# Kernel tuning notes

Hardware: AMD Instinct MI355X
Metric: run time of the kernel (lower is better)

## Reference

```python
import jax, jax.numpy as jnp
import numpy as np

N_HEADS = 16

def setup_inputs() -> dict:
    key = jax.random.key(0)
    k1, k2, k3 = jax.random.split(key, 3)
    B, T, C = 4, 2048, 1024
    x = jax.random.normal(k1, (B, T, C), dtype=jnp.float32)
    tok_mask = jnp.ones((B, T), dtype=bool)
    # weights pre-transposed to [in, out] (torch Linear stores [out, in])
    w_qkv = jax.random.normal(k2, (C, 3 * C), dtype=jnp.float32) * (C ** -0.5)
    w_proj = jax.random.normal(k3, (C, C), dtype=jnp.float32) * (C ** -0.5)
    return {"x": x, "tok_mask": tok_mask, "w_qkv": w_qkv, "w_proj": w_proj}


def reference(x, tok_mask, w_qkv, w_proj):
    B, T, C = x.shape
    H = N_HEADS
    d = C // H
    qkv = x @ w_qkv  # [B, T, 3C]
    q, k, v = jnp.split(qkv, 3, axis=-1)
    # [B, T, C] -> [B, H, T, d]
    def heads(t):
        return t.reshape(B, T, H, d).transpose(0, 2, 1, 3)
    q, k, v = heads(q), heads(k), heads(v)
    att = jnp.einsum('bhtd,bhsd->bhts', q, k) / jnp.sqrt(jnp.float32(d))
    mask = tok_mask[:, None, None, :]  # [B,1,1,T] masks keys
    causal = jnp.tril(jnp.ones((T, T), dtype=bool))[None, None]
    mask = mask & causal
    att = jnp.where(mask, att, jnp.float32(-1e9))
    att = jax.nn.softmax(att, axis=-1)
    # dropout p=0.0 -> identity (eval mode)
    y = jnp.einsum('bhts,bhsd->bhtd', att, v)  # [B,H,T,d]
    y = y.transpose(0, 2, 1, 3).reshape(B, T, C)
    return y @ w_proj
```

## Files before the change

kernel.cpp:

```cpp
#include <hip/hip_runtime.h>
#include <hip/hip_bf16.h>

typedef __attribute__((ext_vector_type(8))) short bf16x8;
typedef __attribute__((ext_vector_type(4))) float f32x4;
typedef __attribute__((ext_vector_type(8))) unsigned short u16x8;
typedef __attribute__((ext_vector_type(2))) unsigned int u32x2;

static constexpr int Tn = 2048;
static constexpr int Cc = 1024;

__device__ __forceinline__ unsigned short f2bf(float f) {
    union { float f; unsigned u; } v; v.f = f;
    unsigned u = v.u;
    u += 0x7FFFu + ((u >> 16) & 1u);
    return (unsigned short)(u >> 16);
}

__device__ __forceinline__ void gload16(const unsigned short* g, unsigned short* l) {
    __builtin_amdgcn_global_load_lds(
        (const __attribute__((address_space(1))) unsigned int*)g,
        (__attribute__((address_space(3))) unsigned int*)l, 16, 0, 0);
}

__global__ void cast_f32_bf16(const float* __restrict__ in,
                              unsigned short* __restrict__ out, int n4) {
    int i = blockIdx.x * blockDim.x + threadIdx.x;
    if (i >= n4) return;
    float4 v = ((const float4*)in)[i];
    ushort4 o;
    o.x = f2bf(v.x); o.y = f2bf(v.y); o.z = f2bf(v.z); o.w = f2bf(v.w);
    ((ushort4*)out)[i] = o;
}

__global__ void transpose_cast(const float* __restrict__ in,
                               unsigned short* __restrict__ out, int R, int N) {
    __shared__ float t[32][33];
    int c0 = blockIdx.x * 32, r0 = blockIdx.y * 32;
    int x = threadIdx.x;
    for (int yy = threadIdx.y; yy < 32; yy += 8)
        t[yy][x] = in[(size_t)(r0 + yy) * N + c0 + x];
    __syncthreads();
    for (int yy = threadIdx.y; yy < 32; yy += 8)
        out[(size_t)(c0 + yy) * R + r0 + x] = f2bf(t[x][yy]);
}

__global__ void v_transpose(const unsigned short* __restrict__ qkv,
                            unsigned short* __restrict__ vt) {
    __shared__ unsigned short tile[64][68];
    const int tid = threadIdx.x;
    const int blk = blockIdx.x;
    const int t = blk & 31;
    const int bh = blk >> 5;
    const int b = bh >> 4, h = bh & 15;
    const size_t base = ((size_t)(b * Tn + t * 64)) * 3072 + 2 * Cc + h * 64;
    const int sr = tid >> 3;
    const int dg = (tid & 7) * 8;
    *(u16x8*)&tile[sr][dg]      = *(const u16x8*)&qkv[base + (size_t)sr * 3072 + dg];
    *(u16x8*)&tile[sr + 32][dg] = *(const u16x8*)&qkv[base + (size_t)(sr + 32) * 3072 + dg];
    __syncthreads();
    const int cg = tid & 7;
    const size_t obase = (size_t)bh * 64 * 2048 + (size_t)t * 64;
#pragma unroll
    for (int half = 0; half < 2; ++half) {
        const int d = (tid >> 3) + half * 32;
        u16x8 o;
#pragma unroll
        for (int j = 0; j < 8; ++j) {
            const int sl = 16 * (j & 3) + 2 * cg + (j >> 2);
            o[j] = tile[sl][d];
        }
        *(u16x8*)&vt[obase + (size_t)d * 2048 + cg * 8] = o;
    }
}

template <int OUT_BF16>
__global__ __launch_bounds__(256) void gemm_bt(const unsigned short* __restrict__ A,
                                               const unsigned short* __restrict__ Bt,
                                               void* __restrict__ Cout,
                                               int Mb, int Nb, int Kk) {
    __shared__ alignas(16) unsigned short As[128 * 64];
    __shared__ alignas(16) unsigned short Bs[128 * 64];
    const int tid = threadIdx.x;
    const int lane = tid & 63;
    const int wave = tid >> 6;
    const int wr = wave >> 1, wc = wave & 1;
    const int l15 = lane & 15;
    const int g = lane >> 4;

    const int nb = Mb * Nb;
    const int bid = blockIdx.x;
    const int swz = (bid & 7) * (nb >> 3) + (bid >> 3);
    const int bx = swz % Nb, by = swz / Nb;
    const int brow = by * 128, bcol = bx * 128;
    const int Nn = Nb * 128;

    const int lr = lane >> 3;
    const int sc = 8 * ((lane & 7) ^ lr);
    const unsigned short* Abase = &A[(size_t)(brow + wave * 32 + lr) * Kk + sc];
    const unsigned short* Bbase = &Bt[(size_t)(bcol + wave * 32 + lr) * Kk + sc];

    f32x4 acc[4][4] = {};

    for (int k0 = 0; k0 < Kk; k0 += 64) {
        __syncthreads();
#pragma unroll
        for (int j = 0; j < 4; ++j) {
            gload16(Abase + (size_t)(j * 8) * Kk + k0, &As[(wave * 32 + j * 8) * 64]);
            gload16(Bbase + (size_t)(j * 8) * Kk + k0, &Bs[(wave * 32 + j * 8) * 64]);
        }
        __syncthreads();

#pragma unroll
        for (int dk = 0; dk < 2; ++dk) {
            const int cs = 8 * ((dk * 4 + g) ^ (l15 & 7));
            bf16x8 af[4], bfr[4];
#pragma unroll
            for (int m = 0; m < 4; ++m)
                af[m] = *(const bf16x8*)&As[(wr * 64 + m * 16 + l15) * 64 + cs];
#pragma unroll
            for (int n = 0; n < 4; ++n)
                bfr[n] = *(const bf16x8*)&Bs[(wc * 64 + n * 16 + l15) * 64 + cs];
#pragma unroll
            for (int m = 0; m < 4; ++m)
#pragma unroll
                for (int n = 0; n < 4; ++n)
                    acc[m][n] = __builtin_amdgcn_mfma_f32_16x16x32_bf16(af[m], bfr[n], acc[m][n], 0, 0, 0);
        }
    }

    const float qs = (OUT_BF16 && bcol < 1024) ? 0.18033688011112042f : 1.0f;

#pragma unroll
    for (int m = 0; m < 4; ++m) {
        int row = brow + wr * 64 + m * 16 + g * 4;
#pragma unroll
        for (int n = 0; n < 4; ++n) {
            int col = bcol + wc * 64 + n * 16 + l15;
#pragma unroll
            for (int i = 0; i < 4; ++i) {
                float v = acc[m][n][i];
                if (OUT_BF16)
                    ((unsigned short*)Cout)[(size_t)(row + i) * Nn + col] = f2bf(v * qs);
                else
                    ((float*)Cout)[(size_t)(row + i) * Nn + col] = v;
            }
        }
    }
}

__global__ __launch_bounds__(512) void attn_fwd(const unsigned short* __restrict__ qkv,
                                                const unsigned short* __restrict__ vt,
                                                unsigned short* __restrict__ yb) {
    __shared__ alignas(16) unsigned short Ks[2][4096];
    __shared__ alignas(16) unsigned short Vs[2][4096];
    __shared__ alignas(16) unsigned int   Ps[8][16][34];

    const int tid = threadIdx.x;
    const int lane = tid & 63;
    const int w = tid >> 6;
    const int l15 = lane & 15;
    const int g = lane >> 4;

    const int bid = blockIdx.x;
    const int xcd = bid & 7;
    const int u = bid >> 3;
    const int bh = xcd * 8 + (u & 7);
    const int qb = 15 - (u >> 3);
    const int b = bh >> 4, h = bh & 15;
    const int rb = b * Tn;
    const int q0 = qb * 128;
    const int colQ = h * 64, colK = Cc + h * 64;

    const int kr = lane >> 3;
    const unsigned short* ksrc =
        &qkv[(size_t)(rb + 8 * w + kr) * 3072 + colK + 8 * ((lane & 7) ^ kr)];
    const unsigned short* vsrc =
        &vt[((size_t)bh * 64 + 8 * w + kr) * 2048 + 8 * ((lane & 7) ^ kr)];

    bf16x8 aq[2];
    {
        const unsigned short* qrow = &qkv[(size_t)(rb + q0 + w * 16 + l15) * 3072 + colQ];
        aq[0] = *(const bf16x8*)&qrow[g * 8];
        aq[1] = *(const bf16x8*)&qrow[32 + g * 8];
    }

    f32x4 accy[4] = {};
    float lsum[4] = {0.f, 0.f, 0.f, 0.f};
    const int kswz = 8 * (l15 & 7);

#define ATILE(P, S0, DG) do {                                                     \
    const unsigned short* kb = &Ks[P][0];                                         \
    const unsigned short* vb = &Vs[P][0];                                         \
    f32x4 accs[4] = {};                                                           \
    __builtin_amdgcn_s_setprio(1);                                                \
    _Pragma("unroll")                                                             \
    for (int dk = 0; dk < 2; ++dk) {                                              \
        _Pragma("unroll")                                                         \
        for (int n = 0; n < 4; ++n) {                                             \
            bf16x8 bk = *(const bf16x8*)&kb[(n * 16 + l15) * 64 +                 \
                                            ((dk * 32 + g * 8) ^ kswz)];          \
            accs[n] = __builtin_amdgcn_mfma_f32_16x16x32_bf16(aq[dk], bk, accs[n], 0, 0, 0); \
        }                                                                         \
    }                                                                             \
    __builtin_amdgcn_s_setprio(0);                                                \
    _Pragma("unroll")                                                             \
    for (int i = 0; i < 4; ++i) {                                                 \
        float pe[4];                                                              \
        _Pragma("unroll")                                                         \
        for (int n = 0; n < 4; ++n) {                                             \
            float v = exp2f(accs[n][i]);                                          \
            if (DG) { if ((S0) + n * 16 + l15 > q0 + w * 16 + g * 4 + i) v = 0.f; } \
            pe[n] = v; lsum[i] += v;                                              \
        }                                                                         \
        u32x2 pk;                                                                 \
        asm("v_cvt_pk_bf16_f32 %0, %1, %2" : "=v"(pk.x) : "v"(pe[0]), "v"(pe[1]));\
        asm("v_cvt_pk_bf16_f32 %0, %1, %2" : "=v"(pk.y) : "v"(pe[2]), "v"(pe[3]));\
        *(u32x2*)&Ps[w][g * 4 + i][l15 * 2] = pk;                                 \
    }                                                                             \
    __builtin_amdgcn_s_setprio(1);                                                \
    _Pragma("unroll")                                                             \
    for (int ks = 0; ks < 2; ++ks) {                                              \
        bf16x8 pa = *(const bf16x8*)&Ps[w][l15][ks * 16 + g * 4];                 \
        _Pragma("unroll")                                                         \
        for (int n = 0; n < 4; ++n) {                                             \
            bf16x8 bv = *(const bf16x8*)&vb[(n * 16 + l15) * 64 +                 \
                                            ((ks * 32 + g * 8) ^ kswz)];          \
            accy[n] = __builtin_amdgcn_mfma_f32_16x16x32_bf16(pa, bv, accy[n], 0, 0, 0); \
        }                                                                         \
    }                                                                             \
    __builtin_amdgcn_s_setprio(0);                                                \
} while (0)

    const int nt = 2 * qb + 2;
    const size_t kstep = (size_t)64 * 3072;

    gload16(ksrc, &Ks[0][w * 512]);
    gload16(vsrc, &Vs[0][w * 512]);
    __syncthreads();

    int p = 0;
    for (int t = 0; t < nt - 2; ++t) {
        gload16(ksrc + (size_t)(t + 1) * kstep, &Ks[p ^ 1][w * 512]);
        gload16(vsrc + (size_t)(t + 1) * 64, &Vs[p ^ 1][w * 512]);
        ATILE(p, t * 64, 0);
        __syncthreads();
        p ^= 1;
    }
    {
        const int t = nt - 2;
        gload16(ksrc + (size_t)(t + 1) * kstep, &Ks[p ^ 1][w * 512]);
        gload16(vsrc + (size_t)(t + 1) * 64, &Vs[p ^ 1][w * 512]);
        ATILE(p, t * 64, 1);
        __syncthreads();
        p ^= 1;
        if (w >= 4) {
            ATILE(p, (t + 1) * 64, 1);
        }
    }
#undef ATILE

#pragma unroll
    for (int i = 0; i < 4; ++i) {
        float ls = lsum[i];
#pragma unroll
        for (int off = 1; off < 16; off <<= 1)
            ls += __shfl_xor(ls, off, 64);
        lsum[i] = ls;
    }
#pragma unroll
    for (int n = 0; n < 4; ++n) {
#pragma unroll
        for (int i = 0; i < 4; ++i) {
            int row = rb + q0 + w * 16 + g * 4 + i;
            int col = h * 64 + n * 16 + l15;
            yb[(size_t)row * 1024 + col] = f2bf(accy[n][i] / lsum[i]);
        }
    }
}

extern "C" void kernel_launch(void* const* d_in, const int* in_sizes, int n_in,
                              void* d_out, int out_size, void* d_ws, size_t ws_size,
                              hipStream_t stream) {
    const float* x      = (const float*)d_in[0];
    const float* w_qkv  = (const float*)d_in[2];
    const float* w_proj = (const float*)d_in[3];
    float* out = (float*)d_out;

    const int M = 4 * 2048;
    unsigned short* xb     = (unsigned short*)d_ws;
    unsigned short* wqkvT  = xb + (size_t)M * 1024;
    unsigned short* wprojT = wqkvT + (size_t)3072 * 1024;
    unsigned short* qkvb   = wprojT + (size_t)1024 * 1024;
    unsigned short* yb     = qkvb + (size_t)M * 3072;
    unsigned short* vt     = xb;

    {
        int n4 = (M * 1024) / 4;
        cast_f32_bf16<<<(n4 + 255) / 256, 256, 0, stream>>>(x, xb, n4);
    }
    transpose_cast<<<dim3(3072 / 32, 1024 / 32), dim3(32, 8), 0, stream>>>(w_qkv, wqkvT, 1024, 3072);
    transpose_cast<<<dim3(1024 / 32, 1024 / 32), dim3(32, 8), 0, stream>>>(w_proj, wprojT, 1024, 1024);

    gemm_bt<1><<<64 * 24, 256, 0, stream>>>(xb, wqkvT, qkvb, 64, 24, 1024);

    v_transpose<<<2048, 256, 0, stream>>>(qkvb, vt);

    attn_fwd<<<1024, 512, 0, stream>>>(qkvb, vt, yb);

    gemm_bt<0><<<64 * 8, 256, 0, stream>>>(yb, wprojT, out, 64, 8, 1024);
}
```

Measured before the change: 185.2 us.

## Keep P in registers via transposed QK MFMA, merge prep kernels

The attention kernel swaps the QK^T MFMA operands so each lane's S-tile layout matches the A-operand layout for the PV MFMA. The exponentiated probabilities can then be packed straight into registers, with no LDS round trip through the Ps buffer. The V transpose permutation is changed to match the new key ordering, and the row-sum reduction becomes a cheaper cross-group shuffle. The three input cast/transpose kernels are also merged into one launch, and occupancy hints are added. This adds permutation complexity that must stay consistent between the V transpose and the MFMA layouts.

```diff
diff --git a/kernel.cpp b/kernel.cpp
--- a/kernel.cpp
+++ b/kernel.cpp
@@ -4,7 +4,6 @@
 typedef __attribute__((ext_vector_type(8))) short bf16x8;
 typedef __attribute__((ext_vector_type(4))) float f32x4;
 typedef __attribute__((ext_vector_type(8))) unsigned short u16x8;
-typedef __attribute__((ext_vector_type(2))) unsigned int u32x2;
 
 static constexpr int Tn = 2048;
 static constexpr int Cc = 1024;
@@ -22,30 +21,40 @@
         (__attribute__((address_space(3))) unsigned int*)l, 16, 0, 0);
 }
 
-__global__ void cast_f32_bf16(const float* __restrict__ in,
-                              unsigned short* __restrict__ out, int n4) {
-    int i = blockIdx.x * blockDim.x + threadIdx.x;
-    if (i >= n4) return;
-    float4 v = ((const float4*)in)[i];
-    ushort4 o;
-    o.x = f2bf(v.x); o.y = f2bf(v.y); o.z = f2bf(v.z); o.w = f2bf(v.w);
-    ((ushort4*)out)[i] = o;
-}
-
-__global__ void transpose_cast(const float* __restrict__ in,
-                               unsigned short* __restrict__ out, int R, int N) {
+__global__ __launch_bounds__(256) void prep(const float* __restrict__ x,
+                                            const float* __restrict__ w_qkv,
+                                            const float* __restrict__ w_proj,
+                                            unsigned short* __restrict__ xb,
+                                            unsigned short* __restrict__ wqkvT,
+                                            unsigned short* __restrict__ wprojT) {
+    const int blk = blockIdx.x;
+    const int tid = threadIdx.x;
+    if (blk < 8192) {
+        int i = blk * 256 + tid;
+        float4 v = ((const float4*)x)[i];
+        ushort4 o;
+        o.x = f2bf(v.x); o.y = f2bf(v.y); o.z = f2bf(v.z); o.w = f2bf(v.w);
+        ((ushort4*)xb)[i] = o;
+        return;
+    }
     __shared__ float t[32][33];
-    int c0 = blockIdx.x * 32, r0 = blockIdx.y * 32;
-    int x = threadIdx.x;
-    for (int yy = threadIdx.y; yy < 32; yy += 8)
-        t[yy][x] = in[(size_t)(r0 + yy) * N + c0 + x];
+    const float* in; unsigned short* out; int R, N, q;
+    if (blk < 11264) { q = blk - 8192;  in = w_qkv;  out = wqkvT;  R = 1024; N = 3072; }
+    else             { q = blk - 11264; in = w_proj; out = wprojT; R = 1024; N = 1024; }
+    const int Nb = N / 32;
+    const int c0 = (q % Nb) * 32, r0 = (q / Nb) * 32;
+    const int xx = tid & 31, y0 = tid >> 5;
+#pragma unroll
+    for (int k = 0; k < 4; ++k)
+        t[y0 + 8 * k][xx] = in[(size_t)(r0 + y0 + 8 * k) * N + c0 + xx];
     __syncthreads();
-    for (int yy = threadIdx.y; yy < 32; yy += 8)
-        out[(size_t)(c0 + yy) * R + r0 + x] = f2bf(t[x][yy]);
-}
-
-__global__ void v_transpose(const unsigned short* __restrict__ qkv,
-                            unsigned short* __restrict__ vt) {
+#pragma unroll
+    for (int k = 0; k < 4; ++k)
+        out[(size_t)(c0 + y0 + 8 * k) * R + r0 + xx] = f2bf(t[xx][y0 + 8 * k]);
+}
+
+__global__ __launch_bounds__(256) void v_transpose(const unsigned short* __restrict__ qkv,
+                                                   unsigned short* __restrict__ vt) {
     __shared__ unsigned short tile[64][68];
     const int tid = threadIdx.x;
     const int blk = blockIdx.x;
@@ -66,7 +75,8 @@
         u16x8 o;
 #pragma unroll
         for (int j = 0; j < 8; ++j) {
-            const int sl = 16 * (j & 3) + 2 * cg + (j >> 2);
+            const int c = cg * 8 + j;
+            const int sl = (c & 32) | ((c & 4) << 2) | ((c & 24) >> 1) | (c & 3);
             o[j] = tile[sl][d];
         }
         *(u16x8*)&vt[obase + (size_t)d * 2048 + cg * 8] = o;
@@ -148,12 +158,11 @@
     }
 }
 
-__global__ __launch_bounds__(512) void attn_fwd(const unsigned short* __restrict__ qkv,
-                                                const unsigned short* __restrict__ vt,
-                                                unsigned short* __restrict__ yb) {
+__global__ __launch_bounds__(512, 4) void attn_fwd(const unsigned short* __restrict__ qkv,
+                                                   const unsigned short* __restrict__ vt,
+                                                   unsigned short* __restrict__ yb) {
     __shared__ alignas(16) unsigned short Ks[2][4096];
     __shared__ alignas(16) unsigned short Vs[2][4096];
-    __shared__ alignas(16) unsigned int   Ps[8][16][34];
 
     const int tid = threadIdx.x;
     const int lane = tid & 63;
@@ -185,8 +194,9 @@
     }
 
     f32x4 accy[4] = {};
-    float lsum[4] = {0.f, 0.f, 0.f, 0.f};
+    float lsum = 0.f;
     const int kswz = 8 * (l15 & 7);
+    const int qglob = q0 + w * 16 + l15;
 
 #define ATILE(P, S0, DG) do {                                                     \
     const unsigned short* kb = &Ks[P][0];                                         \
@@ -199,36 +209,38 @@
         for (int n = 0; n < 4; ++n) {                                             \
             bf16x8 bk = *(const bf16x8*)&kb[(n * 16 + l15) * 64 +                 \
                                             ((dk * 32 + g * 8) ^ kswz)];          \
-            accs[n] = __builtin_amdgcn_mfma_f32_16x16x32_bf16(aq[dk], bk, accs[n], 0, 0, 0); \
+            accs[n] = __builtin_amdgcn_mfma_f32_16x16x32_bf16(bk, aq[dk], accs[n], 0, 0, 0); \
         }                                                                         \
     }                                                                             \
     __builtin_amdgcn_s_setprio(0);                                                \
     _Pragma("unroll")                                                             \
-    for (int i = 0; i < 4; ++i) {                                                 \
-        float pe[4];                                                              \
+    for (int a = 0; a < 2; ++a) {                                                 \
+        float pe[2][4];                                                           \
         _Pragma("unroll")                                                         \
-        for (int n = 0; n < 4; ++n) {                                             \
-            float v = exp2f(accs[n][i]);                                          \
-            if (DG) { if ((S0) + n * 16 + l15 > q0 + w * 16 + g * 4 + i) v = 0.f; } \
-            pe[n] = v; lsum[i] += v;                                              \
+        for (int bb = 0; bb < 2; ++bb) {                                          \
+            const int n = 2 * a + bb;                                             \
+            _Pragma("unroll")                                                     \
+            for (int i = 0; i < 4; ++i) {                                         \
+                float v = exp2f(accs[n][i]);                                      \
+                if (DG) { const int sl = 32 * a + 16 * bb + 4 * g + i;            \
+                          if ((S0) + sl > qglob) v = 0.f; }                       \
+                pe[bb][i] = v; lsum += v;                                         \
+            }                                                                     \
         }                                                                         \
-        u32x2 pk;                                                                 \
-        asm("v_cvt_pk_bf16_f32 %0, %1, %2" : "=v"(pk.x) : "v"(pe[0]), "v"(pe[1]));\
-        asm("v_cvt_pk_bf16_f32 %0, %1, %2" : "=v"(pk.y) : "v"(pe[2]), "v"(pe[3]));\
-        *(u32x2*)&Ps[w][g * 4 + i][l15 * 2] = pk;                                 \
-    }                                                                             \
-    __builtin_amdgcn_s_setprio(1);                                                \
-    _Pragma("unroll")                                                             \
-    for (int ks = 0; ks < 2; ++ks) {                                              \
-        bf16x8 pa = *(const bf16x8*)&Ps[w][l15][ks * 16 + g * 4];                 \
+        union { unsigned uu[4]; bf16x8 v8; } pa;                                  \
+        asm("v_cvt_pk_bf16_f32 %0, %1, %2" : "=v"(pa.uu[0]) : "v"(pe[0][0]), "v"(pe[0][1])); \
+        asm("v_cvt_pk_bf16_f32 %0, %1, %2" : "=v"(pa.uu[1]) : "v"(pe[0][2]), "v"(pe[0][3])); \
+        asm("v_cvt_pk_bf16_f32 %0, %1, %2" : "=v"(pa.uu[2]) : "v"(pe[1][0]), "v"(pe[1][1])); \
+        asm("v_cvt_pk_bf16_f32 %0, %1, %2" : "=v"(pa.uu[3]) : "v"(pe[1][2]), "v"(pe[1][3])); \
+        __builtin_amdgcn_s_setprio(1);                                            \
         _Pragma("unroll")                                                         \
         for (int n = 0; n < 4; ++n) {                                             \
             bf16x8 bv = *(const bf16x8*)&vb[(n * 16 + l15) * 64 +                 \
-                                            ((ks * 32 + g * 8) ^ kswz)];          \
-            accy[n] = __builtin_amdgcn_mfma_f32_16x16x32_bf16(pa, bv, accy[n], 0, 0, 0); \
+                                            ((a * 32 + g * 8) ^ kswz)];           \
+            accy[n] = __builtin_amdgcn_mfma_f32_16x16x32_bf16(pa.v8, bv, accy[n], 0, 0, 0); \
         }                                                                         \
+        __builtin_amdgcn_s_setprio(0);                                            \
     }                                                                             \
-    __builtin_amdgcn_s_setprio(0);                                                \
 } while (0)
 
     const int nt = 2 * qb + 2;
@@ -259,21 +271,19 @@
     }
 #undef ATILE
 
-#pragma unroll
-    for (int i = 0; i < 4; ++i) {
-        float ls = lsum[i];
-#pragma unroll
-        for (int off = 1; off < 16; off <<= 1)
-            ls += __shfl_xor(ls, off, 64);
-        lsum[i] = ls;
-    }
+    lsum += __shfl_xor(lsum, 16, 64);
+    lsum += __shfl_xor(lsum, 32, 64);
+    float ls[4];
+#pragma unroll
+    for (int i = 0; i < 4; ++i)
+        ls[i] = __shfl(lsum, g * 4 + i, 64);
 #pragma unroll
     for (int n = 0; n < 4; ++n) {
 #pragma unroll
         for (int i = 0; i < 4; ++i) {
             int row = rb + q0 + w * 16 + g * 4 + i;
             int col = h * 64 + n * 16 + l15;
-            yb[(size_t)row * 1024 + col] = f2bf(accy[n][i] / lsum[i]);
+            yb[(size_t)row * 1024 + col] = f2bf(accy[n][i] / ls[i]);
         }
     }
 }
@@ -294,12 +304,7 @@
     unsigned short* yb     = qkvb + (size_t)M * 3072;
     unsigned short* vt     = xb;
 
-    {
-        int n4 = (M * 1024) / 4;
-        cast_f32_bf16<<<(n4 + 255) / 256, 256, 0, stream>>>(x, xb, n4);
-    }
-    transpose_cast<<<dim3(3072 / 32, 1024 / 32), dim3(32, 8), 0, stream>>>(w_qkv, wqkvT, 1024, 3072);
-    transpose_cast<<<dim3(1024 / 32, 1024 / 32), dim3(32, 8), 0, stream>>>(w_proj, wprojT, 1024, 1024);
+    prep<<<12288, 256, 0, stream>>>(x, w_qkv, w_proj, xb, wqkvT, wprojT);
 
     gemm_bt<1><<<64 * 24, 256, 0, stream>>>(xb, wqkvT, qkvb, 64, 24, 1024);
 
```

Result: faster. 167.9 us, median of 2 (-9.3%).
